# Kernel tuning notes

Hardware: AMD Instinct MI355X
Metric: run time of the kernel (lower is better)

Reference implementation:

```python
import jax, jax.numpy as jnp
import numpy as np

INIT_L = 512.0
EPS = 1e-6
N_HEAD = 16


def fire_bias(T, w1, b1, w2, b2, c, L_multiplier):
    # positions and relative distances
    pos = jnp.arange(T, dtype=jnp.float32)
    rel = pos[:, None] - pos[None, :]                      # (T, T)
    threshold = jnp.abs(L_multiplier * INIT_L)
    pos_norm = jnp.maximum(pos, threshold)[:, None]        # (T, 1)
    rel = jnp.log(jnp.abs(c * rel) + 1.0)                  # (T, T)
    pos_norm = jnp.log(jnp.abs(c * pos_norm) + 1.0) + EPS  # (T, 1)
    nd = rel / pos_norm                                    # (T, T)
    # tiny MLP: 1 -> mlp_width -> n_head
    h = jax.nn.relu(nd[..., None] * w1[0] + b1)            # (T, T, 32)
    bias = jnp.einsum('tsw,wh->hts', h, w2) + b2[:, None, None]  # (H, T, T)
    causal = jnp.tril(jnp.ones((T, T), dtype=bool))
    bias = jnp.where(causal[None], bias, -jnp.inf)
    return bias[None]                                      # (1, H, T, T)


def reference(x, Wqkv, bqkv, Wproj, bproj, w1, b1, w2, b2, c_param, L_multiplier):
    B, T, C = x.shape
    H = N_HEAD
    hd = C // H
    qkv = x @ Wqkv + bqkv                                  # (B, T, 3C)
    q, k, v = jnp.split(qkv, 3, axis=-1)
    q = q.reshape(B, T, H, hd).transpose(0, 2, 1, 3)       # (B, H, T, hd)
    k = k.reshape(B, T, H, hd).transpose(0, 2, 1, 3)
    v = v.reshape(B, T, H, hd).transpose(0, 2, 1, 3)
    bias = fire_bias(T, w1, b1, w2, b2, c_param, L_multiplier)  # (1, H, T, T)
    scale = 1.0 / jnp.sqrt(jnp.float32(hd))
    att = jnp.einsum('bhqd,bhkd->bhqk', q, k) * scale + bias
    att = jax.nn.softmax(att, axis=-1)
    y = jnp.einsum('bhqk,bhkd->bhqd', att, v)              # (B, H, T, hd)
    y = y.transpose(0, 2, 1, 3).reshape(B, T, C)
    return y @ Wproj + bproj


def setup_inputs() -> dict:
    key = jax.random.key(0)
    ks = jax.random.split(key, 8)
    B, T, C, H, W = 2, 2048, 1024, 16, 32
    s = 0.02
    return {
        'x': jax.random.normal(ks[0], (B, T, C), jnp.float32),
        'Wqkv': jax.random.normal(ks[1], (C, 3 * C), jnp.float32) * s,
        'bqkv': jnp.zeros((3 * C,), jnp.float32),
        'Wproj': jax.random.normal(ks[2], (C, C), jnp.float32) * s,
        'bproj': jnp.zeros((C,), jnp.float32),
        'w1': jax.random.normal(ks[3], (1, W), jnp.float32),
        'b1': jnp.zeros((W,), jnp.float32),
        'w2': jax.random.normal(ks[4], (W, H), jnp.float32) * 0.1,
        'b2': jnp.zeros((H,), jnp.float32),
        'c_param': jnp.float32(0.1),
        'L_multiplier': jnp.float32(1.0),
    }
```

## Files before the change

kernel.cpp:

```cpp
#include <hip/hip_runtime.h>
#include <cstdint>

typedef unsigned short u16;
typedef unsigned int u32;

typedef short bf16x8 __attribute__((ext_vector_type(8)));
typedef float f32x4 __attribute__((ext_vector_type(4)));

#define LN2 0.69314718055994530942f
#define LOG2E 1.44269504088896340736f
#define INFF __builtin_inff()

__device__ __forceinline__ u16 f2bf(float f) {
  u32 u = __float_as_uint(f);
  u = (u + 0x7fffu + ((u >> 16) & 1u)) >> 16;
  return (u16)u;
}
__device__ __forceinline__ u16 f2bfr(float f) {
  return (u16)((__float_as_uint(f) + 0x8000u) >> 16);
}


__global__ void k_convert_x(const float* __restrict__ in, u16* __restrict__ out, int n4) {
  int i = blockIdx.x * blockDim.x + threadIdx.x;
  if (i < n4) {
    float4 v = ((const float4*)in)[i];
    ushort4 o;
    o.x = f2bf(v.x); o.y = f2bf(v.y); o.z = f2bf(v.z); o.w = f2bf(v.w);
    ((ushort4*)out)[i] = o;
  }
}

__global__ void k_transpose_bf(const float* __restrict__ in, u16* __restrict__ out, int R, int C) {
  __shared__ float t[32][33];
  int c0 = blockIdx.x * 32, r0 = blockIdx.y * 32;
  int tx = threadIdx.x, ty = threadIdx.y;
#pragma unroll
  for (int k = 0; k < 4; k++) t[ty + 8 * k][tx] = in[(size_t)(r0 + ty + 8 * k) * C + c0 + tx];
  __syncthreads();
#pragma unroll
  for (int k = 0; k < 4; k++) out[(size_t)(c0 + ty + 8 * k) * R + r0 + tx] = f2bf(t[tx][ty + 8 * k]);
}

__global__ void k_tables(const float* __restrict__ cP, const float* __restrict__ lP,
                         float* __restrict__ ig2, float* __restrict__ rl) {
  int t = blockIdx.x * blockDim.x + threadIdx.x;
  float c = fabsf(cP[0]);
  if (t < 2048) {
    float lm = lP[0];
    float thr = fabsf(lm * 512.0f);
    float pn = fmaxf((float)t, thr);
    float den = logf(c * pn + 1.0f) + 1e-6f;
    ig2[t] = LN2 / den;
  }
  if (t < 2112) {
    int d = t - 63;
    if (d < 0) d = 0;
    rl[t] = log2f(c * (float)d + 1.0f);
  }
}

__global__ void k_segments(const float* __restrict__ w1, const float* __restrict__ b1,
                           const float* __restrict__ w2, const float* __restrict__ b2,
                           float* __restrict__ segX, float* __restrict__ segA,
                           float* __restrict__ segB, int* __restrict__ segU) {
  __shared__ float xs[32];
  __shared__ float srt[32];
  __shared__ float uniq[32];
  __shared__ int uCnt;
  int t = threadIdx.x;
  if (t < 32) {
    float w = w1[t], b = b1[t];
    xs[t] = (w != 0.0f) ? (-b / w) : INFF;
  }
  __syncthreads();
  if (t < 32) {
    float x = xs[t];
    int r = 0;
    for (int v = 0; v < 32; v++) {
      float xv = xs[v];
      if (xv < x || (xv == x && v < t)) r++;
    }
    srt[r] = x;
  }
  __syncthreads();
  if (t == 0) {
    int u = 0;
    for (int i = 0; i < 32; i++) {
      float v = srt[i];
      if (v < 3.0e38f && (u == 0 || v != uniq[u - 1])) uniq[u++] = v;
    }
    uCnt = u;
    segU[0] = u;
  }
  __syncthreads();
  int u = uCnt;
  if (t < u) segX[t] = uniq[t];
  for (int idx = t; idx < (u + 1) * 16; idx += blockDim.x) {
    int j = idx >> 4, h = idx & 15;
    float p;
    if (u == 0) p = 0.0f;
    else if (j == 0) p = uniq[0] - 1.0f;
    else if (j == u) p = uniq[u - 1] + 1.0f;
    else p = 0.5f * (uniq[j - 1] + uniq[j]);
    float A = b2[h], B = 0.0f;
    for (int w = 0; w < 32; w++) {
      float w1w = w1[w], b1w = b1[w], w2wh = w2[w * 16 + h];
      if (w1w != 0.0f) {
        if (fmaf(w1w, p, b1w) > 0.0f) { B += w1w * w2wh; A += b1w * w2wh; }
      } else if (b1w > 0.0f) {
        A += b1w * w2wh;
      }
    }
    segA[j * 16 + h] = A;
    segB[j * 16 + h] = B;
  }
}

template <int MODE>
__launch_bounds__(256, 3)
__global__ void k_gemm(const u16* __restrict__ A, const u16* __restrict__ BT,
                       const float* __restrict__ bias, float* __restrict__ outF,
                       u16* __restrict__ outQ, u16* __restrict__ outK, u16* __restrict__ outV,
                       int M, int N, int K) {
  __shared__ u16 As[128][72];
  __shared__ u16 Bs[128][72];
  const int tid = threadIdx.x;
  const int lane = tid & 63, wave = tid >> 6;
  const int li = lane & 15, quad = lane >> 4;
  const int wrow = (wave >> 1) * 64, wcol = (wave & 1) * 64;
  const int rb = blockIdx.y * 128, cb = blockIdx.x * 128;
  const int srow = tid >> 1, shalf = tid & 1;

  f32x4 acc[4][4];
#pragma unroll
  for (int i = 0; i < 4; i++)
#pragma unroll
    for (int j = 0; j < 4; j++) acc[i][j] = (f32x4){0.f, 0.f, 0.f, 0.f};

  const u16* gA = A + (size_t)(rb + srow) * K + shalf * 32;
  const u16* gB = BT + (size_t)(cb + srow) * K + shalf * 32;

  for (int k0 = 0; k0 < K; k0 += 64) {
    uint4 a0 = *(const uint4*)(gA + k0);
    uint4 a1 = *(const uint4*)(gA + k0 + 8);
    uint4 a2 = *(const uint4*)(gA + k0 + 16);
    uint4 a3 = *(const uint4*)(gA + k0 + 24);
    uint4 b0 = *(const uint4*)(gB + k0);
    uint4 b1 = *(const uint4*)(gB + k0 + 8);
    uint4 b2v = *(const uint4*)(gB + k0 + 16);
    uint4 b3 = *(const uint4*)(gB + k0 + 24);
    __syncthreads();
    *(uint4*)(&As[srow][shalf * 32]) = a0;
    *(uint4*)(&As[srow][shalf * 32 + 8]) = a1;
    *(uint4*)(&As[srow][shalf * 32 + 16]) = a2;
    *(uint4*)(&As[srow][shalf * 32 + 24]) = a3;
    *(uint4*)(&Bs[srow][shalf * 32]) = b0;
    *(uint4*)(&Bs[srow][shalf * 32 + 8]) = b1;
    *(uint4*)(&Bs[srow][shalf * 32 + 16]) = b2v;
    *(uint4*)(&Bs[srow][shalf * 32 + 24]) = b3;
    __syncthreads();
#pragma unroll
    for (int c = 0; c < 2; c++) {
      bf16x8 af[4], bfr[4];
#pragma unroll
      for (int mt = 0; mt < 4; mt++)
        af[mt] = *(const bf16x8*)(&As[wrow + mt * 16 + li][c * 32 + quad * 8]);
#pragma unroll
      for (int nt = 0; nt < 4; nt++)
        bfr[nt] = *(const bf16x8*)(&Bs[wcol + nt * 16 + li][c * 32 + quad * 8]);
#pragma unroll
      for (int mt = 0; mt < 4; mt++)
#pragma unroll
        for (int nt = 0; nt < 4; nt++)
          acc[mt][nt] = __builtin_amdgcn_mfma_f32_16x16x32_bf16(af[mt], bfr[nt], acc[mt][nt], 0, 0, 0);
    }
  }

#pragma unroll
  for (int mt = 0; mt < 4; mt++)
#pragma unroll
    for (int nt = 0; nt < 4; nt++)
#pragma unroll
      for (int r = 0; r < 4; r++) {
        int row = rb + wrow + mt * 16 + quad * 4 + r;
        int col = cb + wcol + nt * 16 + li;
        float v = acc[mt][nt][r] + bias[col];
        if (MODE == 0) {
          int b = row >> 11, tt = row & 2047;
          int sel = col >> 10, w = col & 1023, h = w >> 6, dd = w & 63;
          u16* dst = (sel == 0) ? outQ : ((sel == 1) ? outK : outV);
          dst[(size_t)((b * 16 + h) * 2048 + tt) * 64 + dd] = f2bf(v);
        } else {
          outF[(size_t)row * N + col] = v;
        }
      }
}

__launch_bounds__(256, 2)
__global__ void k_attn(const u16* __restrict__ Q, const u16* __restrict__ K,
                       const u16* __restrict__ V, u16* __restrict__ Y,
                       const float* __restrict__ ig2, const float* __restrict__ RL,
                       const float* __restrict__ segX, const float* __restrict__ segA,
                       const float* __restrict__ segB, const int* __restrict__ segU) {
  __shared__ u16 Ks[2][64][72];
  __shared__ u16 Vts[2][64][72];
  __shared__ u16 Ps[64][72];
  __shared__ float rls[2112];
  __shared__ float sXl[32];
  __shared__ float sAl[33];
  __shared__ float sBl[33];

  const int pr = blockIdx.x, h = blockIdx.y, b = blockIdx.z;
  const int tid = threadIdx.x, lane = tid & 63, wave = tid >> 6;
  const int li = lane & 15, quad = lane >> 4;
  const int bh = b * 16 + h;
  const u16* Qg = Q + (size_t)bh * 2048 * 64;
  const u16* Kg = K + (size_t)bh * 2048 * 64;
  const u16* Vg = V + (size_t)bh * 2048 * 64;

  for (int i = tid; i < 2112; i += 256) rls[i] = RL[i];

  const int u = segU[0];
  float x0 = INFF, A0, B0, A1, B1;
  A0 = segA[h]; B0 = segB[h]; A1 = A0; B1 = B0;
  if (u == 1) { x0 = segX[0]; A1 = segA[16 + h]; B1 = segB[16 + h]; }
  if (u > 1) {
    if (tid < u) sXl[tid] = segX[tid];
    if (tid < u + 1) { sAl[tid] = segA[tid * 16 + h]; sBl[tid] = segB[tid * 16 + h]; }
  }
  const float A0e = A0 * LOG2E, A1e = A1 * LOG2E;
  const float SCL = 0.125f * LOG2E;

  auto run_tile = [&](int qt) {
    const int qw = qt * 64 + wave * 16;
    bf16x8 qf[2];
#pragma unroll
    for (int c = 0; c < 2; c++)
      qf[c] = *(const bf16x8*)(Qg + (size_t)(qw + li) * 64 + c * 32 + quad * 8);

    int ti[4];
    float gI[4], x0r[4], B0g[4], B1g[4], mrow[4], lrow[4];
#pragma unroll
    for (int r = 0; r < 4; r++) {
      ti[r] = qw + quad * 4 + r;
      gI[r] = ig2[ti[r]];
      x0r[r] = x0 / gI[r];
      B0g[r] = B0 * gI[r] * LOG2E;
      B1g[r] = B1 * gI[r] * LOG2E;
      mrow[r] = -INFF;
      lrow[r] = 0.0f;
    }
    f32x4 oacc[4];
#pragma unroll
    for (int nt = 0; nt < 4; nt++) oacc[nt] = (f32x4){0.f, 0.f, 0.f, 0.f};

    uint4 kv0, kv1, w0, w1;
    {
      const u16* ksrc = Kg + (size_t)(tid >> 2) * 64 + (tid & 3) * 16;
      kv0 = *(const uint4*)(ksrc);
      kv1 = *(const uint4*)(ksrc + 8);
      const u16* vsrc = Vg + (size_t)(2 * (tid & 31)) * 64 + (tid >> 5) * 8;
      w0 = *(const uint4*)(vsrc);
      w1 = *(const uint4*)(vsrc + 64);
    }
    __syncthreads();

    for (int kt = 0; kt <= qt; kt++) {
      const int kb = kt * 64, buf = kt & 1;
      *(uint4*)(&Ks[buf][tid >> 2][(tid & 3) * 16]) = kv0;
      *(uint4*)(&Ks[buf][tid >> 2][(tid & 3) * 16 + 8]) = kv1;
      {
        const int kkp = tid & 31, d0 = (tid >> 5) * 8;
        const u16* pw0 = (const u16*)&w0;
        const u16* pw1 = (const u16*)&w1;
#pragma unroll
        for (int j = 0; j < 8; j++)
          *(u32*)(&Vts[buf][d0 + j][2 * kkp]) = (u32)pw0[j] | ((u32)pw1[j] << 16);
      }
      __syncthreads();
      if (kt < qt) {
        const u16* ksrc = Kg + (size_t)(kb + 64 + (tid >> 2)) * 64 + (tid & 3) * 16;
        kv0 = *(const uint4*)(ksrc);
        kv1 = *(const uint4*)(ksrc + 8);
        const u16* vsrc = Vg + (size_t)(kb + 64 + 2 * (tid & 31)) * 64 + (tid >> 5) * 8;
        w0 = *(const uint4*)(vsrc);
        w1 = *(const uint4*)(vsrc + 64);
      }

      f32x4 sacc[4];
#pragma unroll
      for (int nt = 0; nt < 4; nt++) sacc[nt] = (f32x4){0.f, 0.f, 0.f, 0.f};
#pragma unroll
      for (int c = 0; c < 2; c++)
#pragma unroll
        for (int nt = 0; nt < 4; nt++) {
          bf16x8 kf = *(const bf16x8*)(&Ks[buf][nt * 16 + li][c * 32 + quad * 8]);
          sacc[nt] = __builtin_amdgcn_mfma_f32_16x16x32_bf16(qf[c], kf, sacc[nt], 0, 0, 0);
        }

      if (u <= 1) {
#pragma unroll
        for (int r = 0; r < 4; r++) {
          const int base = ti[r] - kb - li + 63;
#pragma unroll
          for (int nt = 0; nt < 4; nt++) {
            float rlv = rls[base - nt * 16];
            bool hi = rlv > x0r[r];
            float z = fmaf(rlv, hi ? B1g[r] : B0g[r], hi ? A1e : A0e);
            z = fmaf(sacc[nt][r], SCL, z);
            sacc[nt][r] = (kb + nt * 16 + li > ti[r]) ? -INFF : z;
          }
        }
      } else {
#pragma unroll
        for (int r = 0; r < 4; r++) {
          const int base = ti[r] - kb - li + 63;
#pragma unroll
          for (int nt = 0; nt < 4; nt++) {
            float nd = rls[base - nt * 16] * gI[r];
            int j = 0;
            for (int i = 0; i < u; i++) j += (nd > sXl[i]) ? 1 : 0;
            float z = (fmaf(nd, sBl[j], sAl[j]) + sacc[nt][r] * 0.125f) * LOG2E;
            sacc[nt][r] = (kb + nt * 16 + li > ti[r]) ? -INFF : z;
          }
        }
      }

#pragma unroll
      for (int r = 0; r < 4; r++) {
        float vm = fmaxf(fmaxf(sacc[0][r], sacc[1][r]), fmaxf(sacc[2][r], sacc[3][r]));
#pragma unroll
        for (int off = 1; off < 16; off <<= 1) vm = fmaxf(vm, __shfl_xor(vm, off, 64));
        float mnew = fmaxf(mrow[r], vm);
        float alpha = __builtin_amdgcn_exp2f(mrow[r] - mnew);
        mrow[r] = mnew;
        float s = 0.0f;
#pragma unroll
        for (int nt = 0; nt < 4; nt++) {
          float p = __builtin_amdgcn_exp2f(sacc[nt][r] - mnew);
          sacc[nt][r] = p;
          s += p;
        }
#pragma unroll
        for (int off = 1; off < 16; off <<= 1) s += __shfl_xor(s, off, 64);
        lrow[r] = lrow[r] * alpha + s;
#pragma unroll
        for (int nt = 0; nt < 4; nt++) oacc[nt][r] *= alpha;
      }

#pragma unroll
      for (int nt = 0; nt < 4; nt++)
#pragma unroll
        for (int r = 0; r < 4; r++)
          Ps[wave * 16 + quad * 4 + r][nt * 16 + li] = f2bfr(sacc[nt][r]);

#pragma unroll
      for (int c = 0; c < 2; c++) {
        bf16x8 pf = *(const bf16x8*)(&Ps[wave * 16 + li][c * 32 + quad * 8]);
#pragma unroll
        for (int nt = 0; nt < 4; nt++) {
          bf16x8 vf = *(const bf16x8*)(&Vts[buf][nt * 16 + li][c * 32 + quad * 8]);
          oacc[nt] = __builtin_amdgcn_mfma_f32_16x16x32_bf16(pf, vf, oacc[nt], 0, 0, 0);
        }
      }
    }

#pragma unroll
    for (int r = 0; r < 4; r++) {
      float inv = 1.0f / lrow[r];
      u16* dst = Y + (size_t)(b * 2048 + ti[r]) * 1024 + h * 64;
#pragma unroll
      for (int nt = 0; nt < 4; nt++) dst[nt * 16 + li] = f2bfr(oacc[nt][r] * inv);
    }
  };

  run_tile(pr);
  run_tile(31 - pr);
}

extern "C" void kernel_launch(void* const* d_in, const int* in_sizes, int n_in,
                              void* d_out, int out_size, void* d_ws, size_t ws_size,
                              hipStream_t stream) {
  (void)in_sizes; (void)n_in; (void)out_size; (void)ws_size;
  const float* x = (const float*)d_in[0];
  const float* Wqkv = (const float*)d_in[1];
  const float* bqkv = (const float*)d_in[2];
  const float* Wproj = (const float*)d_in[3];
  const float* bproj = (const float*)d_in[4];
  const float* w1 = (const float*)d_in[5];
  const float* b1 = (const float*)d_in[6];
  const float* w2 = (const float*)d_in[7];
  const float* b2 = (const float*)d_in[8];
  const float* cP = (const float*)d_in[9];
  const float* lP = (const float*)d_in[10];

  char* ws = (char*)d_ws;
  u16* Xbf = (u16*)(ws);
  u16* WqkvT = (u16*)(ws + (size_t)(8 << 20));
  u16* WprojT = (u16*)(ws + (size_t)(14 << 20));
  u16* Qb = (u16*)(ws + (size_t)(16 << 20));
  u16* Kb = (u16*)(ws + (size_t)(24 << 20));
  u16* Vb = (u16*)(ws + (size_t)(32 << 20));
  u16* Yb = (u16*)(ws + (size_t)(40 << 20));
  float* IG = (float*)(ws + (size_t)(48 << 20));
  float* RL = IG + 2048;
  float* SEGX = RL + 2112;
  float* SEGA = SEGX + 32;
  float* SEGB = SEGA + 33 * 16;
  int* SEGU = (int*)(SEGB + 33 * 16);

  k_convert_x<<<4096, 256, 0, stream>>>(x, Xbf, 1048576);
  k_transpose_bf<<<dim3(96, 32), dim3(32, 8), 0, stream>>>(Wqkv, WqkvT, 1024, 3072);
  k_transpose_bf<<<dim3(32, 32), dim3(32, 8), 0, stream>>>(Wproj, WprojT, 1024, 1024);
  k_tables<<<9, 256, 0, stream>>>(cP, lP, IG, RL);
  k_segments<<<1, 64, 0, stream>>>(w1, b1, w2, b2, SEGX, SEGA, SEGB, SEGU);

  k_gemm<0><<<dim3(24, 32), 256, 0, stream>>>(Xbf, WqkvT, bqkv, nullptr, Qb, Kb, Vb,
                                              4096, 3072, 1024);
  k_attn<<<dim3(16, 16, 2), 256, 0, stream>>>(Qb, Kb, Vb, Yb, IG, RL, SEGX, SEGA, SEGB, SEGU);
  k_gemm<1><<<dim3(8, 32), 256, 0, stream>>>(Yb, WprojT, bproj, (float*)d_out, nullptr, nullptr,
                                             nullptr, 4096, 1024, 1024);
}
```

Measured before the change: 256.3 us.

## Use direct global-to-LDS loads in GEMM and transpose attention MFMA layout

The GEMM main loop now fills shared memory with global_load_lds builtins instead of staging tiles through registers, using an unpadded 64-wide LDS layout. The attention kernel swaps the MFMA operand order so each lane owns one query row. Row-max and row-sum reductions then need two cross-quad shuffles instead of four per row, and the causal mask is applied only on the diagonal tile. P and output stores are packed into 64-bit writes. The unpadded LDS layout may cause bank conflicts on fragment reads, and the GEMM loses register-level overlap of loads with compute.

```diff
diff --git a/kernel.cpp b/kernel.cpp
--- a/kernel.cpp
+++ b/kernel.cpp
@@ -19,6 +19,21 @@
 __device__ __forceinline__ u16 f2bfr(float f) {
   return (u16)((__float_as_uint(f) + 0x8000u) >> 16);
 }
+__device__ __forceinline__ u32 pack2bf(float a, float b) {
+  u32 ta = __float_as_uint(a) + 0x8000u;
+  u32 tb = __float_as_uint(b) + 0x8000u;
+  return __builtin_amdgcn_perm(tb, ta, 0x07060302u);
+}
+
+#if __has_builtin(__builtin_amdgcn_global_load_lds)
+#define HAVE_GLDS 1
+__device__ __forceinline__ void glds16(const u16* g, u16* l) {
+  __builtin_amdgcn_global_load_lds((const __attribute__((address_space(1))) void*)g,
+                                   (__attribute__((address_space(3))) void*)l, 16, 0, 0);
+}
+#else
+#define HAVE_GLDS 0
+#endif
 
 
 __global__ void k_convert_x(const float* __restrict__ in, u16* __restrict__ out, int n4) {
@@ -123,6 +138,51 @@
                        const float* __restrict__ bias, float* __restrict__ outF,
                        u16* __restrict__ outQ, u16* __restrict__ outK, u16* __restrict__ outV,
                        int M, int N, int K) {
+#if HAVE_GLDS
+  __shared__ u16 As[128 * 64];
+  __shared__ u16 Bs[128 * 64];
+  const int tid = threadIdx.x;
+  const int lane = tid & 63, wave = tid >> 6;
+  const int li = lane & 15, quad = lane >> 4;
+  const int wrow = (wave >> 1) * 64, wcol = (wave & 1) * 64;
+  const int rb = blockIdx.y * 128, cb = blockIdx.x * 128;
+
+  f32x4 acc[4][4];
+#pragma unroll
+  for (int i = 0; i < 4; i++)
+#pragma unroll
+    for (int j = 0; j < 4; j++) acc[i][j] = (f32x4){0.f, 0.f, 0.f, 0.f};
+
+  const u16* gA = A + (size_t)(rb + (tid >> 3)) * K + (tid & 7) * 8;
+  const u16* gB = BT + (size_t)(cb + (tid >> 3)) * K + (tid & 7) * 8;
+  u16* lA = As + wave * 512;
+  u16* lB = Bs + wave * 512;
+
+  for (int k0 = 0; k0 < K; k0 += 64) {
+    __syncthreads();
+#pragma unroll
+    for (int ch = 0; ch < 4; ch++) {
+      glds16(gA + (size_t)ch * 32 * K + k0, lA + ch * 2048);
+      glds16(gB + (size_t)ch * 32 * K + k0, lB + ch * 2048);
+    }
+    __syncthreads();
+#pragma unroll
+    for (int c = 0; c < 2; c++) {
+      bf16x8 af[4], bfr[4];
+#pragma unroll
+      for (int mt = 0; mt < 4; mt++)
+        af[mt] = *(const bf16x8*)(&As[(wrow + mt * 16 + li) * 64 + c * 32 + quad * 8]);
+#pragma unroll
+      for (int nt = 0; nt < 4; nt++)
+        bfr[nt] = *(const bf16x8*)(&Bs[(wcol + nt * 16 + li) * 64 + c * 32 + quad * 8]);
+#pragma unroll
+      for (int mt = 0; mt < 4; mt++)
+#pragma unroll
+        for (int nt = 0; nt < 4; nt++)
+          acc[mt][nt] = __builtin_amdgcn_mfma_f32_16x16x32_bf16(af[mt], bfr[nt], acc[mt][nt], 0, 0, 0);
+    }
+  }
+#else
   __shared__ u16 As[128][72];
   __shared__ u16 Bs[128][72];
   const int tid = threadIdx.x;
@@ -176,6 +236,7 @@
           acc[mt][nt] = __builtin_amdgcn_mfma_f32_16x16x32_bf16(af[mt], bfr[nt], acc[mt][nt], 0, 0, 0);
     }
   }
+#endif
 
 #pragma unroll
   for (int mt = 0; mt < 4; mt++)
@@ -234,23 +295,16 @@
 
   auto run_tile = [&](int qt) {
     const int qw = qt * 64 + wave * 16;
+    const int t = qw + li;
     bf16x8 qf[2];
 #pragma unroll
     for (int c = 0; c < 2; c++)
-      qf[c] = *(const bf16x8*)(Qg + (size_t)(qw + li) * 64 + c * 32 + quad * 8);
-
-    int ti[4];
-    float gI[4], x0r[4], B0g[4], B1g[4], mrow[4], lrow[4];
-#pragma unroll
-    for (int r = 0; r < 4; r++) {
-      ti[r] = qw + quad * 4 + r;
-      gI[r] = ig2[ti[r]];
-      x0r[r] = x0 / gI[r];
-      B0g[r] = B0 * gI[r] * LOG2E;
-      B1g[r] = B1 * gI[r] * LOG2E;
-      mrow[r] = -INFF;
-      lrow[r] = 0.0f;
-    }
+      qf[c] = *(const bf16x8*)(Qg + (size_t)t * 64 + c * 32 + quad * 8);
+
+    const float gI = ig2[t];
+    const float x0r = x0 / gI;
+    const float B0g = B0 * gI * LOG2E, B1g = B1 * gI * LOG2E;
+    float mrow = -INFF, lrow = 0.0f;
     f32x4 oacc[4];
 #pragma unroll
     for (int nt = 0; nt < 4; nt++) oacc[nt] = (f32x4){0.f, 0.f, 0.f, 0.f};
@@ -296,64 +350,74 @@
 #pragma unroll
         for (int nt = 0; nt < 4; nt++) {
           bf16x8 kf = *(const bf16x8*)(&Ks[buf][nt * 16 + li][c * 32 + quad * 8]);
-          sacc[nt] = __builtin_amdgcn_mfma_f32_16x16x32_bf16(qf[c], kf, sacc[nt], 0, 0, 0);
+          sacc[nt] = __builtin_amdgcn_mfma_f32_16x16x32_bf16(kf, qf[c], sacc[nt], 0, 0, 0);
         }
 
+      const int Cbase = t - kb - quad * 4 + 63;
+      const float* rp = &rls[Cbase - 51];
       if (u <= 1) {
-#pragma unroll
-        for (int r = 0; r < 4; r++) {
-          const int base = ti[r] - kb - li + 63;
-#pragma unroll
-          for (int nt = 0; nt < 4; nt++) {
-            float rlv = rls[base - nt * 16];
-            bool hi = rlv > x0r[r];
-            float z = fmaf(rlv, hi ? B1g[r] : B0g[r], hi ? A1e : A0e);
+        const int lim = Cbase - 63;
+#pragma unroll
+        for (int nt = 0; nt < 4; nt++)
+#pragma unroll
+          for (int r = 0; r < 4; r++) {
+            float rlv = rp[51 - nt * 16 - r];
+            bool hi = rlv > x0r;
+            float z = fmaf(rlv, hi ? B1g : B0g, hi ? A1e : A0e);
             z = fmaf(sacc[nt][r], SCL, z);
-            sacc[nt][r] = (kb + nt * 16 + li > ti[r]) ? -INFF : z;
+            if (kt == qt) z = (nt * 16 + r > lim) ? -INFF : z;
+            sacc[nt][r] = z;
           }
-        }
       } else {
-#pragma unroll
-        for (int r = 0; r < 4; r++) {
-          const int base = ti[r] - kb - li + 63;
-#pragma unroll
-          for (int nt = 0; nt < 4; nt++) {
-            float nd = rls[base - nt * 16] * gI[r];
+        const int lim = Cbase - 63;
+#pragma unroll
+        for (int nt = 0; nt < 4; nt++)
+#pragma unroll
+          for (int r = 0; r < 4; r++) {
+            float nd = rp[51 - nt * 16 - r] * gI;
             int j = 0;
             for (int i = 0; i < u; i++) j += (nd > sXl[i]) ? 1 : 0;
             float z = (fmaf(nd, sBl[j], sAl[j]) + sacc[nt][r] * 0.125f) * LOG2E;
-            sacc[nt][r] = (kb + nt * 16 + li > ti[r]) ? -INFF : z;
+            if (kt == qt) z = (nt * 16 + r > lim) ? -INFF : z;
+            sacc[nt][r] = z;
           }
-        }
-      }
-
-#pragma unroll
-      for (int r = 0; r < 4; r++) {
-        float vm = fmaxf(fmaxf(sacc[0][r], sacc[1][r]), fmaxf(sacc[2][r], sacc[3][r]));
-#pragma unroll
-        for (int off = 1; off < 16; off <<= 1) vm = fmaxf(vm, __shfl_xor(vm, off, 64));
-        float mnew = fmaxf(mrow[r], vm);
-        float alpha = __builtin_amdgcn_exp2f(mrow[r] - mnew);
-        mrow[r] = mnew;
-        float s = 0.0f;
-#pragma unroll
-        for (int nt = 0; nt < 4; nt++) {
+      }
+
+      float vm = -INFF;
+#pragma unroll
+      for (int nt = 0; nt < 4; nt++)
+#pragma unroll
+        for (int r = 0; r < 4; r++) vm = fmaxf(vm, sacc[nt][r]);
+      vm = fmaxf(vm, __shfl_xor(vm, 16, 64));
+      vm = fmaxf(vm, __shfl_xor(vm, 32, 64));
+      float mnew = fmaxf(mrow, vm);
+      float alpha = __builtin_amdgcn_exp2f(mrow - mnew);
+      mrow = mnew;
+      float s = 0.0f;
+#pragma unroll
+      for (int nt = 0; nt < 4; nt++)
+#pragma unroll
+        for (int r = 0; r < 4; r++) {
           float p = __builtin_amdgcn_exp2f(sacc[nt][r] - mnew);
           sacc[nt][r] = p;
           s += p;
         }
-#pragma unroll
-        for (int off = 1; off < 16; off <<= 1) s += __shfl_xor(s, off, 64);
-        lrow[r] = lrow[r] * alpha + s;
-#pragma unroll
-        for (int nt = 0; nt < 4; nt++) oacc[nt][r] *= alpha;
-      }
-
+      s += __shfl_xor(s, 16, 64);
+      s += __shfl_xor(s, 32, 64);
+      lrow = lrow * alpha + s;
 #pragma unroll
       for (int nt = 0; nt < 4; nt++)
 #pragma unroll
-        for (int r = 0; r < 4; r++)
-          Ps[wave * 16 + quad * 4 + r][nt * 16 + li] = f2bfr(sacc[nt][r]);
+        for (int r = 0; r < 4; r++) oacc[nt][r] *= alpha;
+
+      const int prow = wave * 16 + li;
+#pragma unroll
+      for (int nt = 0; nt < 4; nt++) {
+        uint2 pk;
+        pk.x = pack2bf(sacc[nt][0], sacc[nt][1]);
+        pk.y = pack2bf(sacc[nt][2], sacc[nt][3]);
+        *(uint2*)(&Ps[prow][nt * 16 + quad * 4]) = pk;
+      }
 
 #pragma unroll
       for (int c = 0; c < 2; c++) {
@@ -361,17 +425,19 @@
 #pragma unroll
         for (int nt = 0; nt < 4; nt++) {
           bf16x8 vf = *(const bf16x8*)(&Vts[buf][nt * 16 + li][c * 32 + quad * 8]);
-          oacc[nt] = __builtin_amdgcn_mfma_f32_16x16x32_bf16(pf, vf, oacc[nt], 0, 0, 0);
+          oacc[nt] = __builtin_amdgcn_mfma_f32_16x16x32_bf16(vf, pf, oacc[nt], 0, 0, 0);
         }
       }
     }
 
-#pragma unroll
-    for (int r = 0; r < 4; r++) {
-      float inv = 1.0f / lrow[r];
-      u16* dst = Y + (size_t)(b * 2048 + ti[r]) * 1024 + h * 64;
-#pragma unroll
-      for (int nt = 0; nt < 4; nt++) dst[nt * 16 + li] = f2bfr(oacc[nt][r] * inv);
+    float inv = 1.0f / lrow;
+    u16* dst = Y + (size_t)(b * 2048 + t) * 1024 + h * 64 + quad * 4;
+#pragma unroll
+    for (int nt = 0; nt < 4; nt++) {
+      uint2 pk;
+      pk.x = pack2bf(oacc[nt][0] * inv, oacc[nt][1] * inv);
+      pk.y = pack2bf(oacc[nt][2] * inv, oacc[nt][3] * inv);
+      *(uint2*)(dst + nt * 16) = pk;
     }
   };
 
```

New measurement: 243.5 us. 1.05x faster.
